# Optimization experiments

Hardware: AMD Instinct MI355X
Metric: run time of the kernel (lower is better)

## Reference

```python
import jax, jax.numpy as jnp
import numpy as np

B, L, W, M, NL = 8, 2048, 32, 16, 4  # batch, seq len, width, modes, num_layers


def setup_inputs() -> dict:
    key = jax.random.key(0)
    ks = jax.random.split(key, 16)
    u = lambda k, s: jax.random.uniform(k, s, dtype=jnp.float32)
    n = lambda k, s, sc=0.05: jax.random.normal(k, s, dtype=jnp.float32) * sc
    return {
        "x": jax.random.normal(ks[0], (B, L, 1), dtype=jnp.float32),
        "t": jnp.linspace(0.0, 1.0, L, dtype=jnp.float32),  # grid_x_train
        "fc0_w": n(ks[1], (W, 2), 0.5), "fc0_b": n(ks[2], (W,), 0.1),
        # PR params (torch.rand cfloat -> uniform[0,1) real & imag)
        "pole_re": u(ks[3], (NL, W, W, M)), "pole_im": u(ks[4], (NL, W, W, M)),
        "res_re": u(ks[5], (NL, W, W, M)), "res_im": u(ks[6], (NL, W, W, M)),
        # SpectralConv1d params
        "spec_re": u(ks[7], (NL, W, W, M)), "spec_im": u(ks[8], (NL, W, W, M)),
        # 1x1 Conv1d params
        "conv_w": n(ks[9], (NL, W, W)), "conv_b": n(ks[10], (NL, W), 0.01),
        "fc1_w": n(ks[11], (128, W)), "fc1_b": n(ks[12], (128,), 0.01),
        "fc2_w": n(ks[13], (1, 128)), "fc2_b": n(ks[14], (1,), 0.01),
    }


def reference(x, t, fc0_w, fc0_b, pole_re, pole_im, res_re, res_im,
              spec_re, spec_im, conv_w, conv_b, fc1_w, fc1_b, fc2_w, fc2_b):
    Bx, Lx, _ = x.shape
    gelu = lambda v: jax.nn.gelu(v, approximate=False)
    # get_grid + fc0 + gelu, then (B, L, W) -> (B, W, L)
    grid = jnp.broadcast_to(jnp.linspace(0.0, 1.0, Lx, dtype=x.dtype)[None, :, None], (Bx, Lx, 1))
    h = gelu(jnp.concatenate([x, grid], axis=-1) @ fc0_w.T + fc0_b)
    h = jnp.transpose(h, (0, 2, 1))  # (B, W, L)

    dt = t[1] - t[0]
    # lambda = fftfreq(L, dt) * 2*pi*1j (purely imaginary)
    freqs = jnp.fft.fftfreq(Lx).astype(x.dtype) / dt * (2.0 * np.pi)  # (L,)
    lam = jax.lax.complex(jnp.zeros_like(freqs), freqs)  # complex64 (L,)

    for i in range(NL):
        # --- PR (pole-residue Laplace) branch ---
        pole = jax.lax.complex(pole_re[i], pole_im[i])  # (in, out, M)
        res = jax.lax.complex(res_re[i], res_im[i])     # (in, out, M)
        alpha = jnp.fft.fft(h, axis=-1)  # (B, in, L) complex
        # broadcast-reduce: (in, out, L, M) -> sum over modes -> (in, out, L)
        Hw = (res[:, :, None, :] / (lam[None, None, :, None] - pole[:, :, None, :])).sum(-1)
        pr = jnp.real(jnp.fft.ifft(jnp.einsum('bix,iox->box', alpha, Hw), n=Lx, axis=-1))
        # --- SpectralConv1d branch ---
        spec_w = jax.lax.complex(spec_re[i], spec_im[i])  # (in, out, M)
        xf = jnp.fft.rfft(h, axis=-1)  # (B, in, L//2+1)
        out_ft = jnp.zeros_like(xf).at[:, :, :M].set(
            jnp.einsum('bix,iox->box', xf[:, :, :M], spec_w))
        sc = jnp.fft.irfft(out_ft, n=Lx, axis=-1)
        # --- 1x1 conv branch ---
        wv = jnp.einsum('bil,oi->bol', h, conv_w[i]) + conv_b[i][None, :, None]
        h = gelu(pr + sc + wv)

    h = jnp.transpose(h, (0, 2, 1))  # (B, L, W)
    h = gelu(h @ fc1_w.T + fc1_b)
    return h @ fc2_w.T + fc2_b  # (B, L, 1)
```

## Files before the change

### kernel.cpp

```cpp
#include <hip/hip_runtime.h>
#include <math.h>

#define NFFT   2048
#define M2     1024
#define LOG2N  11
#define BB     8
#define WW     32
#define MM     16
#define NLAYER 4
#define AST    1032

#define PAD(i) ((i) + ((i) >> 5))
#define PADDED_M (M2 + (M2 >> 5))

__device__ __forceinline__ float gelu_f(float v) {
    float ax = fabsf(v) * 0.70710678118654752440f;
    float t  = __builtin_amdgcn_rcpf(fmaf(0.3275911f, ax, 1.0f));
    float s  = fmaf(1.061405429f, t, -1.453152027f);
    s = fmaf(s, t, 1.421413741f);
    s = fmaf(s, t, -0.284496736f);
    s = fmaf(s, t, 0.254829592f);
    s = s * t;
    float e  = __expf(-ax * ax);
    float er = fmaf(-s, e, 1.0f);
    er = copysignf(er, v);
    return 0.5f * v * (1.0f + er);
}

__device__ __forceinline__ float2 cadd(float2 a, float2 b) { return make_float2(a.x + b.x, a.y + b.y); }
__device__ __forceinline__ float2 csub(float2 a, float2 b) { return make_float2(a.x - b.x, a.y - b.y); }
__device__ __forceinline__ float2 cmul(float2 a, float2 b) {
    return make_float2(fmaf(a.x, b.x, -a.y * b.y), fmaf(a.x, b.y, a.y * b.x));
}
template<int S> __device__ __forceinline__ float2 caddi(float2 a, float2 b) {
    return (S > 0) ? make_float2(a.x - b.y, a.y + b.x) : make_float2(a.x + b.y, a.y - b.x);
}
template<int S> __device__ __forceinline__ float2 csubi(float2 a, float2 b) {
    return (S > 0) ? make_float2(a.x + b.y, a.y - b.x) : make_float2(a.x - b.y, a.y + b.x);
}

template<int S> __device__ __forceinline__ void dft4(float2* a) {
    float2 t0 = cadd(a[0], a[2]), t1 = csub(a[0], a[2]);
    float2 t2 = cadd(a[1], a[3]), t3 = csub(a[1], a[3]);
    a[0] = cadd(t0, t2);
    a[2] = csub(t0, t2);
    a[1] = caddi<S>(t1, t3);
    a[3] = csubi<S>(t1, t3);
}

template<int LS, int S>
__device__ __forceinline__ void pass_cx(const float2* src, float2* dst, int t, float2 w1f) {
    float2 a[4];
    #pragma unroll
    for (int r = 0; r < 4; ++r) a[r] = src[PAD(t + r * 256)];
    if (LS > 1) {
        float2 w1 = (S > 0) ? make_float2(w1f.x, -w1f.y) : w1f;
        float2 w2 = cmul(w1, w1);
        float2 w3 = cmul(w2, w1);
        a[1] = cmul(a[1], w1);
        a[2] = cmul(a[2], w2);
        a[3] = cmul(a[3], w3);
    }
    dft4<S>(a);
    int s = t & (LS - 1);
    int base = (t / LS) * (4 * LS) + s;
    #pragma unroll
    for (int r = 0; r < 4; ++r) dst[PAD(base + r * LS)] = a[r];
}

struct Tw { float2 t4, t16, t64, t256; };
__device__ __forceinline__ Tw make_tw(int t) {
    Tw w;
    float sn, cs;
    const float c0 = 6.2831853071795864769f;
    __sincosf(c0 * (float)(t & 3)   * (1.0f / 16.0f),   &sn, &cs); w.t4   = make_float2(cs, -sn);
    __sincosf(c0 * (float)(t & 15)  * (1.0f / 64.0f),   &sn, &cs); w.t16  = make_float2(cs, -sn);
    __sincosf(c0 * (float)(t & 63)  * (1.0f / 256.0f),  &sn, &cs); w.t64  = make_float2(cs, -sn);
    __sincosf(c0 * (float)(t & 255) * (1.0f / 1024.0f), &sn, &cs); w.t256 = make_float2(cs, -sn);
    return w;
}

template<int S>
__device__ __forceinline__ void fft1024_cx(float2* A, float2* B, int t, bool act, const Tw& w) {
    if (act) pass_cx<1,   S>(A, B, t, make_float2(1.0f, 0.0f));
    __syncthreads();
    if (act) pass_cx<4,   S>(B, A, t, w.t4);
    __syncthreads();
    if (act) pass_cx<16,  S>(A, B, t, w.t16);
    __syncthreads();
    if (act) pass_cx<64,  S>(B, A, t, w.t64);
    __syncthreads();
    if (act) pass_cx<256, S>(A, B, t, w.t256);
    __syncthreads();
}

__global__ __launch_bounds__(256) void k_genG_fc0(
    const float* __restrict__ pole_re, const float* __restrict__ pole_im,
    const float* __restrict__ res_re,  const float* __restrict__ res_im,
    const float* __restrict__ spec_re, const float* __restrict__ spec_im,
    const float* __restrict__ conv_w,  const float* __restrict__ tgrid,
    const float* __restrict__ x,       const float* __restrict__ fc0_w,
    const float* __restrict__ fc0_b,
    float2* __restrict__ G, float2* __restrict__ alpha)
{
    __shared__ float2 Acx[PADDED_M], Bcx[PADDED_M];
    int t = threadIdx.x;
    int blk = blockIdx.x;
    float dt = tgrid[1] - tgrid[0];
    float fscale = 6.2831853071795864769f / ((float)NFFT * dt);

    if (blk < NLAYER * WW * WW / 4) {
        int lane = t & 63;
        int u = blk * 4 + (t >> 6);
        int l = u >> 10, r = u & 1023, o = r >> 5, i = r & 31;
        int pb = ((l * WW + i) * WW + o) * MM;
        float cw = conv_w[(l * WW + o) * WW + i];
        float w2r[16];
        float2 acc[16];
        #pragma unroll
        for (int j = 0; j < 16; ++j) {
            float wv = fscale * (float)(lane + 64 * j);
            w2r[j] = wv * wv;
            acc[j] = make_float2(cw, 0.0f);
        }
        #pragma unroll
        for (int mq = 0; mq < 4; ++mq) {
            float4 P_re = *(const float4*)&pole_re[pb + 4 * mq];
            float4 P_im = *(const float4*)&pole_im[pb + 4 * mq];
            float4 R_re = *(const float4*)&res_re [pb + 4 * mq];
            float4 R_im = *(const float4*)&res_im [pb + 4 * mq];
            #pragma unroll
            for (int mm = 0; mm < 4; ++mm) {
                float Rp = (&P_re.x)[mm], Ip = (&P_im.x)[mm];
                float Rr = (&R_re.x)[mm], Ir = (&R_im.x)[mm];
                float b   = fmaf(Rr, Rp, Ir * Ip);
                float c   = fmaf(Rp, Rp, Ip * Ip);
                float dd  = 2.0f * Rp;
                float dd2 = dd * dd;
                float add = Rr * dd;
                float bdd = b * dd;
                #pragma unroll
                for (int j = 0; j < 16; ++j) {
                    float uu  = c - w2r[j];
                    float inv = __builtin_amdgcn_rcpf(fmaf(dd2, w2r[j], uu * uu));
                    acc[j].x = fmaf(fmaf(add, w2r[j], b * uu), -inv, acc[j].x);
                    acc[j].y = fmaf(fmaf(Rr, uu, -bdd), inv, acc[j].y);
                }
            }
        }
        #pragma unroll
        for (int j = 0; j < 16; ++j)
            acc[j].y *= fscale * (float)(lane + 64 * j);
        if (lane < MM) {
            if (lane) {
                acc[0].x += spec_re[pb + lane];
                acc[0].y += spec_im[pb + lane];
            } else {
                acc[0].x += spec_re[pb];
            }
        }
        float2* grow = G + (size_t)((l * WW + o) * WW + i) * AST;
        #pragma unroll
        for (int j = 0; j < 16; ++j) grow[lane + 64 * j] = acc[j];
        if (lane == 0) {
            float wn = -fscale * (float)M2;
            float accn = cw;
            #pragma unroll
            for (int mq = 0; mq < 4; ++mq) {
                float4 P_re = *(const float4*)&pole_re[pb + 4 * mq];
                float4 P_im = *(const float4*)&pole_im[pb + 4 * mq];
                float4 R_re = *(const float4*)&res_re [pb + 4 * mq];
                float4 R_im = *(const float4*)&res_im [pb + 4 * mq];
                #pragma unroll
                for (int mm = 0; mm < 4; ++mm) {
                    float Rp = (&P_re.x)[mm], Ip = (&P_im.x)[mm];
                    float Rr = (&R_re.x)[mm], Ir = (&R_im.x)[mm];
                    float e   = wn - Ip;
                    float num = fmaf(Ir, e, -(Rr * Rp));
                    float den = fmaf(e, e, Rp * Rp);
                    accn += num * __builtin_amdgcn_rcpf(den);
                }
            }
            grow[M2] = make_float2(accn, 0.0f);
        }
    } else {
        int row = blk - NLAYER * WW * WW / 4;
        int b = row >> 5, w = row & 31;
        float w0 = fc0_w[2 * w], w1 = fc0_w[2 * w + 1], b0 = fc0_b[w];
        Tw tw = make_tw(t);
        const float2* x2 = (const float2*)(x + (size_t)b * NFFT);
        #pragma unroll
        for (int j = 0; j < 4; ++j) {
            int n = t + j * 256;
            float2 xv = x2[n];
            float g0 = (float)(2 * n)     * (1.0f / 2047.0f);
            float g1 = (float)(2 * n + 1) * (1.0f / 2047.0f);
            float v0 = gelu_f(fmaf(w0, xv.x, fmaf(w1, g0, b0)));
            float v1 = gelu_f(fmaf(w0, xv.y, fmaf(w1, g1, b0)));
            Acx[PAD(n)] = make_float2(v0, v1);
        }
        __syncthreads();
        fft1024_cx<-1>(Acx, Bcx, t, true, tw);
        float2* arow = alpha + (size_t)row * AST;
        #pragma unroll
        for (int j = 0; j < 4; ++j) {
            int k  = t + j * 256;
            int mk = (M2 - k) & (M2 - 1);
            float2 Zk  = Bcx[PAD(k)];
            float2 Zmk = Bcx[PAD(mk)];
            float2 A  = make_float2(0.5f * (Zk.x + Zmk.x), 0.5f * (Zk.y - Zmk.y));
            float2 Bv = make_float2(0.5f * (Zk.y + Zmk.y), -0.5f * (Zk.x - Zmk.x));
            float ph = (3.1415926535897932385f / (float)M2) * (float)k;
            float sn, cs;
            __sincosf(ph, &sn, &cs);
            float2 e = make_float2(cs, -sn);
            float2 X = cadd(A, cmul(Bv, e));
            arow[k] = X;
            if (k == 0) arow[M2] = make_float2(A.x - Bv.x, 0.0f);
        }
    }
}

template<bool LAST>
__global__ __launch_bounds__(512) void k_apply_fft(
    const float2* __restrict__ alpha, const float2* __restrict__ G,
    const float* __restrict__ conv_b, float2* __restrict__ alpha_next,
    float2* __restrict__ hout, int layer)
{
    __shared__ __align__(16) float2 Ycx[M2 + 2];
    __shared__ float2 Acx[PADDED_M], Bcx[PADDED_M];
    int t = threadIdx.x;
    int row = blockIdx.x;
    int b = row >> 5, o = row & 31;
    const float2* abase = alpha + (size_t)(b * WW) * AST;
    const float2* gbase = G + (size_t)((layer * WW + o) * WW) * AST;
    Tw tw;
    if (t < 256) tw = make_tw(t);

    float2 acc0 = make_float2(0.0f, 0.0f);
    float2 acc1 = make_float2(0.0f, 0.0f);
    #pragma unroll 4
    for (int i = 0; i < 32; ++i) {
        const float4* ar = (const float4*)(abase + (size_t)i * AST);
        const float4* gr = (const float4*)(gbase + (size_t)i * AST);
        float4 av = ar[t];
        float4 gv = gr[t];
        acc0.x = fmaf(av.x, gv.x, fmaf(-av.y, gv.y, acc0.x));
        acc0.y = fmaf(av.x, gv.y, fmaf( av.y, gv.x, acc0.y));
        acc1.x = fmaf(av.z, gv.z, fmaf(-av.w, gv.w, acc1.x));
        acc1.y = fmaf(av.z, gv.w, fmaf( av.w, gv.z, acc1.y));
    }
    if (t < 64) {
        float p = 0.0f;
        if (t < 32)
            p = abase[(size_t)t * AST + M2].x * gbase[(size_t)t * AST + M2].x;
        #pragma unroll
        for (int off = 16; off >= 1; off >>= 1) p += __shfl_xor(p, off);
        if (t == 0) Ycx[M2] = make_float2(p, 0.0f);
    }
    if (t == 0) acc0.x += (float)NFFT * conv_b[layer * WW + o];
    ((float4*)Ycx)[t] = make_float4(acc0.x, acc0.y, acc1.x, acc1.y);
    __syncthreads();

    #pragma unroll
    for (int j = 0; j < 2; ++j) {
        int k = t + j * 512;
        float2 Xk = Ycx[k];
        float2 Xm = Ycx[M2 - k];
        float2 A = make_float2(0.5f * (Xk.x + Xm.x), 0.5f * (Xk.y - Xm.y));
        float2 u = make_float2(Xk.x - Xm.x, Xk.y + Xm.y);
        float ph = (3.1415926535897932385f / (float)M2) * (float)k;
        float sn, cs;
        __sincosf(ph, &sn, &cs);
        float2 e = make_float2(cs, sn);
        float2 Bv = cmul(u, e);
        Acx[PAD(k)] = make_float2(A.x - 0.5f * Bv.y, A.y + 0.5f * Bv.x);
    }
    __syncthreads();
    fft1024_cx<1>(Acx, Bcx, t, t < 256, tw);
    const float invM = 1.0f / (float)M2;
    if (LAST) {
        #pragma unroll
        for (int j = 0; j < 2; ++j) {
            int n = t + j * 512;
            float2 z = Bcx[PAD(n)];
            hout[(size_t)row * M2 + n] = make_float2(gelu_f(z.x * invM), gelu_f(z.y * invM));
        }
    } else {
        #pragma unroll
        for (int j = 0; j < 2; ++j) {
            int n = t + j * 512;
            float2 z = Bcx[PAD(n)];
            Acx[PAD(n)] = make_float2(gelu_f(z.x * invM), gelu_f(z.y * invM));
        }
        __syncthreads();
        fft1024_cx<-1>(Acx, Bcx, t, t < 256, tw);
        float2* arow = alpha_next + (size_t)row * AST;
        #pragma unroll
        for (int j = 0; j < 2; ++j) {
            int k  = t + j * 512;
            int mk = (M2 - k) & (M2 - 1);
            float2 Zk  = Bcx[PAD(k)];
            float2 Zmk = Bcx[PAD(mk)];
            float2 A  = make_float2(0.5f * (Zk.x + Zmk.x), 0.5f * (Zk.y - Zmk.y));
            float2 Bv = make_float2(0.5f * (Zk.y + Zmk.y), -0.5f * (Zk.x - Zmk.x));
            float ph = (3.1415926535897932385f / (float)M2) * (float)k;
            float sn, cs;
            __sincosf(ph, &sn, &cs);
            float2 e = make_float2(cs, -sn);
            float2 X = cadd(A, cmul(Bv, e));
            arow[k] = X;
            if (k == 0) arow[M2] = make_float2(A.x - Bv.x, 0.0f);
        }
    }
}

__global__ __launch_bounds__(256) void k_head(
    const float* __restrict__ h, const float* __restrict__ fc1_w,
    const float* __restrict__ fc1_b, const float* __restrict__ fc2_w,
    const float* __restrict__ fc2_b, float* __restrict__ out)
{
    __shared__ float s_w1[128 * 32];
    __shared__ float s_b1[128];
    __shared__ float s_w2[128];
    __shared__ float s_part[4][64];
    int t = threadIdx.x;
    for (int j = t; j < 128 * 32; j += 256) s_w1[j] = fc1_w[j];
    if (t < 128) { s_b1[t] = fc1_b[t]; s_w2[t] = fc2_w[t]; }
    __syncthreads();
    int wv  = t >> 6;
    int ln  = t & 63;
    int pos = blockIdx.x * 64 + ln;
    int b = pos >> LOG2N, l = pos & (NFFT - 1);
    float hreg[32];
    #pragma unroll
    for (int w = 0; w < 32; ++w) hreg[w] = h[(b * WW + w) * NFFT + l];
    float acc = 0.0f;
    int n0 = wv * 32;
    for (int n = n0; n < n0 + 32; ++n) {
        float a = s_b1[n];
        #pragma unroll
        for (int w = 0; w < 32; w += 4) {
            float4 ww = *(const float4*)&s_w1[n * 32 + w];
            a = fmaf(ww.x, hreg[w],     a);
            a = fmaf(ww.y, hreg[w + 1], a);
            a = fmaf(ww.z, hreg[w + 2], a);
            a = fmaf(ww.w, hreg[w + 3], a);
        }
        acc = fmaf(s_w2[n], gelu_f(a), acc);
    }
    s_part[wv][ln] = acc;
    __syncthreads();
    if (t < 64) {
        float r = s_part[0][t] + s_part[1][t] + s_part[2][t] + s_part[3][t] + fc2_b[0];
        out[blockIdx.x * 64 + t] = r;
    }
}

extern "C" void kernel_launch(void* const* d_in, const int* in_sizes, int n_in,
                              void* d_out, int out_size, void* d_ws, size_t ws_size,
                              hipStream_t stream)
{
    const float* x       = (const float*)d_in[0];
    const float* tg      = (const float*)d_in[1];
    const float* fc0_w   = (const float*)d_in[2];
    const float* fc0_b   = (const float*)d_in[3];
    const float* pole_re = (const float*)d_in[4];
    const float* pole_im = (const float*)d_in[5];
    const float* res_re  = (const float*)d_in[6];
    const float* res_im  = (const float*)d_in[7];
    const float* spec_re = (const float*)d_in[8];
    const float* spec_im = (const float*)d_in[9];
    const float* conv_w  = (const float*)d_in[10];
    const float* conv_b  = (const float*)d_in[11];
    const float* fc1_w   = (const float*)d_in[12];
    const float* fc1_b   = (const float*)d_in[13];
    const float* fc2_w   = (const float*)d_in[14];
    const float* fc2_b   = (const float*)d_in[15];
    float* out = (float*)d_out;

    char* ws = (char*)d_ws;
    const size_t plane = (size_t)(BB * WW) * AST * sizeof(float2);
    float2* alphaA = (float2*)ws;
    float2* alphaB = (float2*)(ws + plane);
    float2* hbuf   = (float2*)(ws + 2 * plane);
    float2* Gbuf   = (float2*)(ws + 3 * plane);

    hipLaunchKernelGGL(k_genG_fc0, dim3(NLAYER * WW * WW / 4 + BB * WW), dim3(256), 0, stream,
                       pole_re, pole_im, res_re, res_im, spec_re, spec_im,
                       conv_w, tg, x, fc0_w, fc0_b, Gbuf, alphaA);
    float2* acur = alphaA;
    float2* anxt = alphaB;
    for (int layer = 0; layer < NLAYER; ++layer) {
        if (layer < NLAYER - 1)
            hipLaunchKernelGGL((k_apply_fft<false>), dim3(BB * WW), dim3(512), 0, stream,
                               acur, Gbuf, conv_b, anxt, (float2*)nullptr, layer);
        else
            hipLaunchKernelGGL((k_apply_fft<true>), dim3(BB * WW), dim3(512), 0, stream,
                               acur, Gbuf, conv_b, (float2*)nullptr, hbuf, layer);
        float2* tmp = acur; acur = anxt; anxt = tmp;
    }
    hipLaunchKernelGGL(k_head, dim3(BB * NFFT / 64), dim3(256), 0, stream,
                       (const float*)hbuf, fc1_w, fc1_b, fc2_w, fc2_b, out);
}
```

Before: 90.96 us.

## Use mixed radix-4/8 FFT with fewer passes and 256-thread apply blocks

Replaces the five radix-4 passes of the 1024-point complex FFT with a radix-4, radix-8, radix-8, radix-4 sequence. This cuts one shared-memory round trip and one barrier per transform and needs one fewer twiddle sincos. The per-layer apply kernel now runs 256 threads per block, each handling two float4 pairs in the complex contraction and four points in the pre- and post-processing. In exchange, half the threads sit idle during the radix-8 passes and each block carries fewer waves to hide memory latency.

```diff
diff --git a/kernel.cpp b/kernel.cpp
--- a/kernel.cpp
+++ b/kernel.cpp
@@ -48,6 +48,32 @@
     a[3] = csubi<S>(t1, t3);
 }
 
+template<int S> __device__ __forceinline__ void dft8(float2* a) {
+    const float c = 0.70710678118654752440f;
+    float2 t0 = cadd(a[0], a[4]), t1 = csub(a[0], a[4]);
+    float2 t2 = cadd(a[2], a[6]), t3 = csub(a[2], a[6]);
+    float2 u0 = cadd(a[1], a[5]), u1 = csub(a[1], a[5]);
+    float2 u2 = cadd(a[3], a[7]), u3 = csub(a[3], a[7]);
+    float2 e0 = cadd(t0, t2), e2 = csub(t0, t2);
+    float2 e1 = caddi<S>(t1, t3), e3 = csubi<S>(t1, t3);
+    float2 o0 = cadd(u0, u2), o2 = csub(u0, u2);
+    float2 o1 = caddi<S>(u1, u3), o3 = csubi<S>(u1, u3);
+    float2 w1o, w2o, w3o;
+    if (S < 0) {
+        w1o = make_float2(c * (o1.x + o1.y), c * (o1.y - o1.x));
+        w2o = make_float2(o2.y, -o2.x);
+        w3o = make_float2(c * (o3.y - o3.x), c * (-o3.y - o3.x));
+    } else {
+        w1o = make_float2(c * (o1.x - o1.y), c * (o1.y + o1.x));
+        w2o = make_float2(-o2.y, o2.x);
+        w3o = make_float2(c * (-o3.x - o3.y), c * (o3.x - o3.y));
+    }
+    a[0] = cadd(e0, o0);  a[4] = csub(e0, o0);
+    a[1] = cadd(e1, w1o); a[5] = csub(e1, w1o);
+    a[2] = cadd(e2, w2o); a[6] = csub(e2, w2o);
+    a[3] = cadd(e3, w3o); a[7] = csub(e3, w3o);
+}
+
 template<int LS, int S>
 __device__ __forceinline__ void pass_cx(const float2* src, float2* dst, int t, float2 w1f) {
     float2 a[4];
@@ -68,29 +94,43 @@
     for (int r = 0; r < 4; ++r) dst[PAD(base + r * LS)] = a[r];
 }
 
-struct Tw { float2 t4, t16, t64, t256; };
-__device__ __forceinline__ Tw make_tw(int t) {
-    Tw w;
+template<int LS, int S>
+__device__ __forceinline__ void pass8_cx(const float2* src, float2* dst, int t, float2 w1f) {
+    float2 a[8];
+    #pragma unroll
+    for (int r = 0; r < 8; ++r) a[r] = src[PAD(t + r * 128)];
+    float2 w1 = (S > 0) ? make_float2(w1f.x, -w1f.y) : w1f;
+    a[1] = cmul(a[1], w1);
+    float2 wr = w1;
+    #pragma unroll
+    for (int r = 2; r < 8; ++r) { wr = cmul(wr, w1); a[r] = cmul(a[r], wr); }
+    dft8<S>(a);
+    int s = t & (LS - 1);
+    int base = (t / LS) * (8 * LS) + s;
+    #pragma unroll
+    for (int r = 0; r < 8; ++r) dst[PAD(base + r * LS)] = a[r];
+}
+
+struct Tw2 { float2 a, b, c; };
+__device__ __forceinline__ Tw2 make_tw2(int t) {
+    Tw2 w;
     float sn, cs;
     const float c0 = 6.2831853071795864769f;
-    __sincosf(c0 * (float)(t & 3)   * (1.0f / 16.0f),   &sn, &cs); w.t4   = make_float2(cs, -sn);
-    __sincosf(c0 * (float)(t & 15)  * (1.0f / 64.0f),   &sn, &cs); w.t16  = make_float2(cs, -sn);
-    __sincosf(c0 * (float)(t & 63)  * (1.0f / 256.0f),  &sn, &cs); w.t64  = make_float2(cs, -sn);
-    __sincosf(c0 * (float)(t & 255) * (1.0f / 1024.0f), &sn, &cs); w.t256 = make_float2(cs, -sn);
+    __sincosf(c0 * (float)(t & 3)   * (1.0f / 32.0f),   &sn, &cs); w.a = make_float2(cs, -sn);
+    __sincosf(c0 * (float)(t & 31)  * (1.0f / 256.0f),  &sn, &cs); w.b = make_float2(cs, -sn);
+    __sincosf(c0 * (float)(t & 255) * (1.0f / 1024.0f), &sn, &cs); w.c = make_float2(cs, -sn);
     return w;
 }
 
 template<int S>
-__device__ __forceinline__ void fft1024_cx(float2* A, float2* B, int t, bool act, const Tw& w) {
-    if (act) pass_cx<1,   S>(A, B, t, make_float2(1.0f, 0.0f));
-    __syncthreads();
-    if (act) pass_cx<4,   S>(B, A, t, w.t4);
-    __syncthreads();
-    if (act) pass_cx<16,  S>(A, B, t, w.t16);
-    __syncthreads();
-    if (act) pass_cx<64,  S>(B, A, t, w.t64);
-    __syncthreads();
-    if (act) pass_cx<256, S>(A, B, t, w.t256);
+__device__ __forceinline__ void fft1024_4p(float2* A, float2* B, int t, const Tw2& w) {
+    pass_cx<1, S>(A, B, t, make_float2(1.0f, 0.0f));
+    __syncthreads();
+    if (t < 128) pass8_cx<4,  S>(B, A, t, w.a);
+    __syncthreads();
+    if (t < 128) pass8_cx<32, S>(A, B, t, w.b);
+    __syncthreads();
+    pass_cx<256, S>(B, A, t, w.c);
     __syncthreads();
 }
 
@@ -187,7 +227,7 @@
         int row = blk - NLAYER * WW * WW / 4;
         int b = row >> 5, w = row & 31;
         float w0 = fc0_w[2 * w], w1 = fc0_w[2 * w + 1], b0 = fc0_b[w];
-        Tw tw = make_tw(t);
+        Tw2 tw = make_tw2(t);
         const float2* x2 = (const float2*)(x + (size_t)b * NFFT);
         #pragma unroll
         for (int j = 0; j < 4; ++j) {
@@ -200,14 +240,14 @@
             Acx[PAD(n)] = make_float2(v0, v1);
         }
         __syncthreads();
-        fft1024_cx<-1>(Acx, Bcx, t, true, tw);
+        fft1024_4p<-1>(Acx, Bcx, t, tw);
         float2* arow = alpha + (size_t)row * AST;
         #pragma unroll
         for (int j = 0; j < 4; ++j) {
             int k  = t + j * 256;
             int mk = (M2 - k) & (M2 - 1);
-            float2 Zk  = Bcx[PAD(k)];
-            float2 Zmk = Bcx[PAD(mk)];
+            float2 Zk  = Acx[PAD(k)];
+            float2 Zmk = Acx[PAD(mk)];
             float2 A  = make_float2(0.5f * (Zk.x + Zmk.x), 0.5f * (Zk.y - Zmk.y));
             float2 Bv = make_float2(0.5f * (Zk.y + Zmk.y), -0.5f * (Zk.x - Zmk.x));
             float ph = (3.1415926535897932385f / (float)M2) * (float)k;
@@ -222,7 +262,7 @@
 }
 
 template<bool LAST>
-__global__ __launch_bounds__(512) void k_apply_fft(
+__global__ __launch_bounds__(256) void k_apply_fft(
     const float2* __restrict__ alpha, const float2* __restrict__ G,
     const float* __restrict__ conv_b, float2* __restrict__ alpha_next,
     float2* __restrict__ hout, int layer)
@@ -234,21 +274,26 @@
     int b = row >> 5, o = row & 31;
     const float2* abase = alpha + (size_t)(b * WW) * AST;
     const float2* gbase = G + (size_t)((layer * WW + o) * WW) * AST;
-    Tw tw;
-    if (t < 256) tw = make_tw(t);
+    Tw2 tw = make_tw2(t);
 
     float2 acc0 = make_float2(0.0f, 0.0f);
     float2 acc1 = make_float2(0.0f, 0.0f);
+    float2 acc2 = make_float2(0.0f, 0.0f);
+    float2 acc3 = make_float2(0.0f, 0.0f);
     #pragma unroll 4
     for (int i = 0; i < 32; ++i) {
         const float4* ar = (const float4*)(abase + (size_t)i * AST);
         const float4* gr = (const float4*)(gbase + (size_t)i * AST);
-        float4 av = ar[t];
-        float4 gv = gr[t];
-        acc0.x = fmaf(av.x, gv.x, fmaf(-av.y, gv.y, acc0.x));
-        acc0.y = fmaf(av.x, gv.y, fmaf( av.y, gv.x, acc0.y));
-        acc1.x = fmaf(av.z, gv.z, fmaf(-av.w, gv.w, acc1.x));
-        acc1.y = fmaf(av.z, gv.w, fmaf( av.w, gv.z, acc1.y));
+        float4 av0 = ar[2 * t], av1 = ar[2 * t + 1];
+        float4 gv0 = gr[2 * t], gv1 = gr[2 * t + 1];
+        acc0.x = fmaf(av0.x, gv0.x, fmaf(-av0.y, gv0.y, acc0.x));
+        acc0.y = fmaf(av0.x, gv0.y, fmaf( av0.y, gv0.x, acc0.y));
+        acc1.x = fmaf(av0.z, gv0.z, fmaf(-av0.w, gv0.w, acc1.x));
+        acc1.y = fmaf(av0.z, gv0.w, fmaf( av0.w, gv0.z, acc1.y));
+        acc2.x = fmaf(av1.x, gv1.x, fmaf(-av1.y, gv1.y, acc2.x));
+        acc2.y = fmaf(av1.x, gv1.y, fmaf( av1.y, gv1.x, acc2.y));
+        acc3.x = fmaf(av1.z, gv1.z, fmaf(-av1.w, gv1.w, acc3.x));
+        acc3.y = fmaf(av1.z, gv1.w, fmaf( av1.w, gv1.z, acc3.y));
     }
     if (t < 64) {
         float p = 0.0f;
@@ -259,12 +304,13 @@
         if (t == 0) Ycx[M2] = make_float2(p, 0.0f);
     }
     if (t == 0) acc0.x += (float)NFFT * conv_b[layer * WW + o];
-    ((float4*)Ycx)[t] = make_float4(acc0.x, acc0.y, acc1.x, acc1.y);
-    __syncthreads();
-
-    #pragma unroll
-    for (int j = 0; j < 2; ++j) {
-        int k = t + j * 512;
+    ((float4*)Ycx)[2 * t]     = make_float4(acc0.x, acc0.y, acc1.x, acc1.y);
+    ((float4*)Ycx)[2 * t + 1] = make_float4(acc2.x, acc2.y, acc3.x, acc3.y);
+    __syncthreads();
+
+    #pragma unroll
+    for (int j = 0; j < 4; ++j) {
+        int k = t + j * 256;
         float2 Xk = Ycx[k];
         float2 Xm = Ycx[M2 - k];
         float2 A = make_float2(0.5f * (Xk.x + Xm.x), 0.5f * (Xk.y - Xm.y));
@@ -277,28 +323,28 @@
         Acx[PAD(k)] = make_float2(A.x - 0.5f * Bv.y, A.y + 0.5f * Bv.x);
     }
     __syncthreads();
-    fft1024_cx<1>(Acx, Bcx, t, t < 256, tw);
+    fft1024_4p<1>(Acx, Bcx, t, tw);
     const float invM = 1.0f / (float)M2;
     if (LAST) {
         #pragma unroll
-        for (int j = 0; j < 2; ++j) {
-            int n = t + j * 512;
-            float2 z = Bcx[PAD(n)];
+        for (int j = 0; j < 4; ++j) {
+            int n = t + j * 256;
+            float2 z = Acx[PAD(n)];
             hout[(size_t)row * M2 + n] = make_float2(gelu_f(z.x * invM), gelu_f(z.y * invM));
         }
     } else {
         #pragma unroll
-        for (int j = 0; j < 2; ++j) {
-            int n = t + j * 512;
-            float2 z = Bcx[PAD(n)];
-            Acx[PAD(n)] = make_float2(gelu_f(z.x * invM), gelu_f(z.y * invM));
+        for (int j = 0; j < 4; ++j) {
+            int n = t + j * 256;
+            float2 z = Acx[PAD(n)];
+            Bcx[PAD(n)] = make_float2(gelu_f(z.x * invM), gelu_f(z.y * invM));
         }
         __syncthreads();
-        fft1024_cx<-1>(Acx, Bcx, t, t < 256, tw);
+        fft1024_4p<-1>(Bcx, Acx, t, tw);
         float2* arow = alpha_next + (size_t)row * AST;
         #pragma unroll
-        for (int j = 0; j < 2; ++j) {
-            int k  = t + j * 512;
+        for (int j = 0; j < 4; ++j) {
+            int k  = t + j * 256;
             int mk = (M2 - k) & (M2 - 1);
             float2 Zk  = Bcx[PAD(k)];
             float2 Zmk = Bcx[PAD(mk)];
@@ -393,10 +439,10 @@
     float2* anxt = alphaB;
     for (int layer = 0; layer < NLAYER; ++layer) {
         if (layer < NLAYER - 1)
-            hipLaunchKernelGGL((k_apply_fft<false>), dim3(BB * WW), dim3(512), 0, stream,
+            hipLaunchKernelGGL((k_apply_fft<false>), dim3(BB * WW), dim3(256), 0, stream,
                                acur, Gbuf, conv_b, anxt, (float2*)nullptr, layer);
         else
-            hipLaunchKernelGGL((k_apply_fft<true>), dim3(BB * WW), dim3(512), 0, stream,
+            hipLaunchKernelGGL((k_apply_fft<true>), dim3(BB * WW), dim3(256), 0, stream,
                                acur, Gbuf, conv_b, (float2*)nullptr, hbuf, layer);
         float2* tmp = acur; acur = anxt; anxt = tmp;
     }
```

Result: slower. 96.55 us (+6.1%).

## Spread per-layer transfer-function generation across the layer apply kernels

Applied to the files above, without the earlier changes.

Instead of generating the G tables for all four layers in the first kernel, only layer 0's table is built up front. Each apply kernel gets 128 extra blocks that build the next layer's G while the main blocks process the current layer. This overlaps the heavy rational-function evaluation with the FFT/apply work and shortens the initial serial kernel. The cost is a larger grid and possible contention between the extra blocks and the apply blocks.

```diff
diff --git a/kernel.cpp b/kernel.cpp
--- a/kernel.cpp
+++ b/kernel.cpp
@@ -92,6 +92,85 @@
     __syncthreads();
     if (act) pass_cx<256, S>(A, B, t, w.t256);
     __syncthreads();
+}
+
+__device__ __forceinline__ void genG_unit(
+    int l, int o, int i, int lane, float fscale,
+    const float* __restrict__ pole_re, const float* __restrict__ pole_im,
+    const float* __restrict__ res_re,  const float* __restrict__ res_im,
+    const float* __restrict__ spec_re, const float* __restrict__ spec_im,
+    const float* __restrict__ conv_w,  float2* __restrict__ G)
+{
+    int pb = ((l * WW + i) * WW + o) * MM;
+    float cw = conv_w[(l * WW + o) * WW + i];
+    float w2r[16];
+    float2 acc[16];
+    #pragma unroll
+    for (int j = 0; j < 16; ++j) {
+        float wv = fscale * (float)(lane + 64 * j);
+        w2r[j] = wv * wv;
+        acc[j] = make_float2(cw, 0.0f);
+    }
+    #pragma unroll
+    for (int mq = 0; mq < 4; ++mq) {
+        float4 P_re = *(const float4*)&pole_re[pb + 4 * mq];
+        float4 P_im = *(const float4*)&pole_im[pb + 4 * mq];
+        float4 R_re = *(const float4*)&res_re [pb + 4 * mq];
+        float4 R_im = *(const float4*)&res_im [pb + 4 * mq];
+        #pragma unroll
+        for (int mm = 0; mm < 4; ++mm) {
+            float Rp = (&P_re.x)[mm], Ip = (&P_im.x)[mm];
+            float Rr = (&R_re.x)[mm], Ir = (&R_im.x)[mm];
+            float b   = fmaf(Rr, Rp, Ir * Ip);
+            float c   = fmaf(Rp, Rp, Ip * Ip);
+            float dd  = 2.0f * Rp;
+            float dd2 = dd * dd;
+            float add = Rr * dd;
+            float bdd = b * dd;
+            #pragma unroll
+            for (int j = 0; j < 16; ++j) {
+                float uu  = c - w2r[j];
+                float inv = __builtin_amdgcn_rcpf(fmaf(dd2, w2r[j], uu * uu));
+                acc[j].x = fmaf(fmaf(add, w2r[j], b * uu), -inv, acc[j].x);
+                acc[j].y = fmaf(fmaf(Rr, uu, -bdd), inv, acc[j].y);
+            }
+        }
+    }
+    #pragma unroll
+    for (int j = 0; j < 16; ++j)
+        acc[j].y *= fscale * (float)(lane + 64 * j);
+    if (lane < MM) {
+        if (lane) {
+            acc[0].x += spec_re[pb + lane];
+            acc[0].y += spec_im[pb + lane];
+        } else {
+            acc[0].x += spec_re[pb];
+        }
+    }
+    float2* grow = G + (size_t)((l * WW + o) * WW + i) * AST;
+    #pragma unroll
+    for (int j = 0; j < 16; ++j) grow[lane + 64 * j] = acc[j];
+    if (lane == 0) {
+        float wn = -fscale * (float)M2;
+        float accn = cw;
+        #pragma unroll
+        for (int mq = 0; mq < 4; ++mq) {
+            float4 P_re = *(const float4*)&pole_re[pb + 4 * mq];
+            float4 P_im = *(const float4*)&pole_im[pb + 4 * mq];
+            float4 R_re = *(const float4*)&res_re [pb + 4 * mq];
+            float4 R_im = *(const float4*)&res_im [pb + 4 * mq];
+            #pragma unroll
+            for (int mm = 0; mm < 4; ++mm) {
+                float Rp = (&P_re.x)[mm], Ip = (&P_im.x)[mm];
+                float Rr = (&R_re.x)[mm], Ir = (&R_im.x)[mm];
+                float e   = wn - Ip;
+                float num = fmaf(Ir, e, -(Rr * Rp));
+                float den = fmaf(e, e, Rp * Rp);
+                accn += num * __builtin_amdgcn_rcpf(den);
+            }
+        }
+        grow[M2] = make_float2(accn, 0.0f);
+    }
 }
 
 __global__ __launch_bounds__(256) void k_genG_fc0(
@@ -109,82 +188,12 @@
     float dt = tgrid[1] - tgrid[0];
     float fscale = 6.2831853071795864769f / ((float)NFFT * dt);
 
-    if (blk < NLAYER * WW * WW / 4) {
-        int lane = t & 63;
+    if (blk < WW * WW / 4) {
         int u = blk * 4 + (t >> 6);
-        int l = u >> 10, r = u & 1023, o = r >> 5, i = r & 31;
-        int pb = ((l * WW + i) * WW + o) * MM;
-        float cw = conv_w[(l * WW + o) * WW + i];
-        float w2r[16];
-        float2 acc[16];
-        #pragma unroll
-        for (int j = 0; j < 16; ++j) {
-            float wv = fscale * (float)(lane + 64 * j);
-            w2r[j] = wv * wv;
-            acc[j] = make_float2(cw, 0.0f);
-        }
-        #pragma unroll
-        for (int mq = 0; mq < 4; ++mq) {
-            float4 P_re = *(const float4*)&pole_re[pb + 4 * mq];
-            float4 P_im = *(const float4*)&pole_im[pb + 4 * mq];
-            float4 R_re = *(const float4*)&res_re [pb + 4 * mq];
-            float4 R_im = *(const float4*)&res_im [pb + 4 * mq];
-            #pragma unroll
-            for (int mm = 0; mm < 4; ++mm) {
-                float Rp = (&P_re.x)[mm], Ip = (&P_im.x)[mm];
-                float Rr = (&R_re.x)[mm], Ir = (&R_im.x)[mm];
-                float b   = fmaf(Rr, Rp, Ir * Ip);
-                float c   = fmaf(Rp, Rp, Ip * Ip);
-                float dd  = 2.0f * Rp;
-                float dd2 = dd * dd;
-                float add = Rr * dd;
-                float bdd = b * dd;
-                #pragma unroll
-                for (int j = 0; j < 16; ++j) {
-                    float uu  = c - w2r[j];
-                    float inv = __builtin_amdgcn_rcpf(fmaf(dd2, w2r[j], uu * uu));
-                    acc[j].x = fmaf(fmaf(add, w2r[j], b * uu), -inv, acc[j].x);
-                    acc[j].y = fmaf(fmaf(Rr, uu, -bdd), inv, acc[j].y);
-                }
-            }
-        }
-        #pragma unroll
-        for (int j = 0; j < 16; ++j)
-            acc[j].y *= fscale * (float)(lane + 64 * j);
-        if (lane < MM) {
-            if (lane) {
-                acc[0].x += spec_re[pb + lane];
-                acc[0].y += spec_im[pb + lane];
-            } else {
-                acc[0].x += spec_re[pb];
-            }
-        }
-        float2* grow = G + (size_t)((l * WW + o) * WW + i) * AST;
-        #pragma unroll
-        for (int j = 0; j < 16; ++j) grow[lane + 64 * j] = acc[j];
-        if (lane == 0) {
-            float wn = -fscale * (float)M2;
-            float accn = cw;
-            #pragma unroll
-            for (int mq = 0; mq < 4; ++mq) {
-                float4 P_re = *(const float4*)&pole_re[pb + 4 * mq];
-                float4 P_im = *(const float4*)&pole_im[pb + 4 * mq];
-                float4 R_re = *(const float4*)&res_re [pb + 4 * mq];
-                float4 R_im = *(const float4*)&res_im [pb + 4 * mq];
-                #pragma unroll
-                for (int mm = 0; mm < 4; ++mm) {
-                    float Rp = (&P_re.x)[mm], Ip = (&P_im.x)[mm];
-                    float Rr = (&R_re.x)[mm], Ir = (&R_im.x)[mm];
-                    float e   = wn - Ip;
-                    float num = fmaf(Ir, e, -(Rr * Rp));
-                    float den = fmaf(e, e, Rp * Rp);
-                    accn += num * __builtin_amdgcn_rcpf(den);
-                }
-            }
-            grow[M2] = make_float2(accn, 0.0f);
-        }
+        genG_unit(0, u >> 5, u & 31, t & 63, fscale,
+                  pole_re, pole_im, res_re, res_im, spec_re, spec_im, conv_w, G);
     } else {
-        int row = blk - NLAYER * WW * WW / 4;
+        int row = blk - WW * WW / 4;
         int b = row >> 5, w = row & 31;
         float w0 = fc0_w[2 * w], w1 = fc0_w[2 * w + 1], b0 = fc0_b[w];
         Tw tw = make_tw(t);
@@ -225,12 +234,28 @@
 __global__ __launch_bounds__(512) void k_apply_fft(
     const float2* __restrict__ alpha, const float2* __restrict__ G,
     const float* __restrict__ conv_b, float2* __restrict__ alpha_next,
-    float2* __restrict__ hout, int layer)
+    float2* __restrict__ hout, int layer,
+    const float* __restrict__ pole_re, const float* __restrict__ pole_im,
+    const float* __restrict__ res_re,  const float* __restrict__ res_im,
+    const float* __restrict__ spec_re, const float* __restrict__ spec_im,
+    const float* __restrict__ conv_w,  const float* __restrict__ tgrid,
+    float2* __restrict__ Gout, int genL)
 {
     __shared__ __align__(16) float2 Ycx[M2 + 2];
     __shared__ float2 Acx[PADDED_M], Bcx[PADDED_M];
     int t = threadIdx.x;
-    int row = blockIdx.x;
+    int blk = blockIdx.x;
+
+    if (blk >= BB * WW) {
+        float dt = tgrid[1] - tgrid[0];
+        float fscale = 6.2831853071795864769f / ((float)NFFT * dt);
+        int u = (blk - BB * WW) * 8 + (t >> 6);
+        genG_unit(genL, u >> 5, u & 31, t & 63, fscale,
+                  pole_re, pole_im, res_re, res_im, spec_re, spec_im, conv_w, Gout);
+        return;
+    }
+
+    int row = blk;
     int b = row >> 5, o = row & 31;
     const float2* abase = alpha + (size_t)(b * WW) * AST;
     const float2* gbase = G + (size_t)((layer * WW + o) * WW) * AST;
@@ -386,18 +411,24 @@
     float2* hbuf   = (float2*)(ws + 2 * plane);
     float2* Gbuf   = (float2*)(ws + 3 * plane);
 
-    hipLaunchKernelGGL(k_genG_fc0, dim3(NLAYER * WW * WW / 4 + BB * WW), dim3(256), 0, stream,
+    hipLaunchKernelGGL(k_genG_fc0, dim3(WW * WW / 4 + BB * WW), dim3(256), 0, stream,
                        pole_re, pole_im, res_re, res_im, spec_re, spec_im,
                        conv_w, tg, x, fc0_w, fc0_b, Gbuf, alphaA);
     float2* acur = alphaA;
     float2* anxt = alphaB;
     for (int layer = 0; layer < NLAYER; ++layer) {
+        int genL = layer + 1;
+        int grid = BB * WW + ((genL < NLAYER) ? 128 : 0);
         if (layer < NLAYER - 1)
-            hipLaunchKernelGGL((k_apply_fft<false>), dim3(BB * WW), dim3(512), 0, stream,
-                               acur, Gbuf, conv_b, anxt, (float2*)nullptr, layer);
+            hipLaunchKernelGGL((k_apply_fft<false>), dim3(grid), dim3(512), 0, stream,
+                               acur, Gbuf, conv_b, anxt, (float2*)nullptr, layer,
+                               pole_re, pole_im, res_re, res_im, spec_re, spec_im,
+                               conv_w, tg, Gbuf, genL);
         else
-            hipLaunchKernelGGL((k_apply_fft<true>), dim3(BB * WW), dim3(512), 0, stream,
-                               acur, Gbuf, conv_b, (float2*)nullptr, hbuf, layer);
+            hipLaunchKernelGGL((k_apply_fft<true>), dim3(grid), dim3(512), 0, stream,
+                               acur, Gbuf, conv_b, (float2*)nullptr, hbuf, layer,
+                               pole_re, pole_im, res_re, res_im, spec_re, spec_im,
+                               conv_w, tg, Gbuf, genL);
         float2* tmp = acur; acur = anxt; anxt = tmp;
     }
     hipLaunchKernelGGL(k_head, dim3(BB * NFFT / 64), dim3(256), 0, stream,
```

Measured after the change: 106.8 us. +17.5%, slower.
